# Performance work log

Hardware: AMD Instinct MI355X
Metric: run time of the kernel (lower is better)

## Reference

```python
import jax, jax.numpy as jnp
import numpy as np


def setup_inputs() -> dict:
    key = jax.random.key(0)
    k1, k2 = jax.random.split(key)
    B, N, M, D = 8, 8192, 8192, 3
    preds = jax.random.normal(k1, (B, M, D), dtype=jnp.float32)
    gts = jax.random.normal(k2, (B, N, D), dtype=jnp.float32)
    return {"preds": preds, "gts": gts}


def reference(preds, gts):
    # Faithful to torch: P = batch_pairwise_dist(x=gts, y=preds), shape [B, N_gts, N_preds]
    x = gts.astype(jnp.float32)
    y = preds.astype(jnp.float32)
    xx = jnp.sum(x * x, axis=-1)                      # [B, N]
    yy = jnp.sum(y * y, axis=-1)                      # [B, M]
    zz = jnp.einsum('bnd,bmd->bnm', x, y)             # [B, N, M]
    P = xx[:, :, None] + yy[:, None, :] - 2.0 * zz    # squared distances
    loss_1 = jnp.mean(jnp.min(P, axis=1))             # min over gts points
    loss_2 = jnp.mean(jnp.min(P, axis=2))             # min over pred points
    return loss_1 + loss_2
```

## Files before the change

### kernel.cpp

```cpp
#include <hip/hip_runtime.h>
#include <hip/hip_bf16.h>


typedef _Float16 f16x8 __attribute__((ext_vector_type(8)));
typedef float f32x16 __attribute__((ext_vector_type(16)));

#define NPTS 8192
#define BATCH 8
#define TPB 512
#define BN 512
#define BM 1024
#define CPB 4
#define CTPC (BM / 32)
#define NQ_TOT (2 * BATCH * NPTS)

__device__ __forceinline__ void cvt_split(float v, _Float16& h, _Float16& l) {
    h = (_Float16)v;
    l = (_Float16)(v - (float)h);
}

__global__ __launch_bounds__(TPB, 4) void chamfer_mfma_kernel(
    const float* __restrict__ preds, const float* __restrict__ gts,
    float* __restrict__ partial )
{
    __shared__ f16x8 ldsB[CTPC][2][32];

    const int bid  = blockIdx.x;
    const int pass = bid >> 8;
    const int b       = (bid >> 5) & 7;
    const int rowblk  = (bid >> 1) & 15;
    const int colhalf = bid & 1;

    const float* __restrict__ Asrc = (pass == 0) ? gts : preds;
    const float* __restrict__ Bsrc = (pass == 0) ? preds : gts;
    const float* __restrict__ Ab = Asrc + (size_t)b * NPTS * 3;
    const float* __restrict__ Bb = Bsrc + (size_t)b * NPTS * 3;

    const int tid  = threadIdx.x;
    const int lane = tid & 63;
    const int w    = tid >> 6;
    const int kh   = lane >> 5;
    const int cl   = lane & 31;

    f16x8 af[2];
#pragma unroll
    for (int t = 0; t < 2; ++t) {
        const int row = rowblk * BN + w * 64 + t * 32 + cl;
        const float* xp = Ab + (size_t)row * 3;
        const float x0 = xp[0], x1 = xp[1], x2 = xp[2];
        _Float16 h0, l0, h1, l1, h2, l2;
        cvt_split(x0, h0, l0); cvt_split(x1, h1, l1); cvt_split(x2, h2, l2);
        const float xx = x0 * x0 + x1 * x1 + x2 * x2;
        _Float16 xxh, xxl; cvt_split(xx, xxh, xxl);
        const f16x8 lo = { h0, h1, h2, l0, l1, l2, h0, h1 };
        const f16x8 hi = { h2, (_Float16)1, (_Float16)1, xxh, xxl,
                           (_Float16)0, (_Float16)0, (_Float16)0 };
        af[t] = kh ? hi : lo;
    }

    const f16x8* __restrict__ bptr = &ldsB[0][kh][cl];
    const f32x16 zc = {};

    float rb[2][16];
#pragma unroll
    for (int t = 0; t < 2; ++t)
#pragma unroll
        for (int r = 0; r < 16; ++r) rb[t][r] = 1e30f;

    for (int chunk = 0; chunk < CPB; ++chunk) {
        const int cbase = (colhalf * CPB + chunk) * BM;
        __syncthreads();
#pragma unroll
        for (int i = 0; i < BM / TPB; ++i) {
            const int pl = i * TPB + tid;
            const float* yp = Bb + (size_t)(cbase + pl) * 3;
            const float y0 = yp[0], y1 = yp[1], y2 = yp[2];
            _Float16 nh0, nl0, nh1, nl1, nh2, nl2;
            { const float hf = (float)(_Float16)y0; nh0 = (_Float16)(-2.f * hf); nl0 = (_Float16)(-2.f * (y0 - hf)); }
            { const float hf = (float)(_Float16)y1; nh1 = (_Float16)(-2.f * hf); nl1 = (_Float16)(-2.f * (y1 - hf)); }
            { const float hf = (float)(_Float16)y2; nh2 = (_Float16)(-2.f * hf); nl2 = (_Float16)(-2.f * (y2 - hf)); }
            const float yy = y0 * y0 + y1 * y1 + y2 * y2;
            _Float16 yyh, yyl; cvt_split(yy, yyh, yyl);
            const f16x8 lo = { nh0, nh1, nh2, nh0, nh1, nh2, nl0, nl1 };
            const f16x8 hi = { nl2, yyh, yyl, (_Float16)1, (_Float16)1,
                               (_Float16)0, (_Float16)0, (_Float16)0 };
            ldsB[pl >> 5][0][pl & 31] = lo;
            ldsB[pl >> 5][1][pl & 31] = hi;
        }
        __syncthreads();

#pragma unroll 2
        for (int ct = 0; ct < CTPC; ct += 2) {
            const f16x8 bfA = bptr[ct * 64];
            const f16x8 bfB = bptr[(ct + 1) * 64];
#pragma unroll
            for (int t = 0; t < 2; ++t) {
                const f32x16 aA = __builtin_amdgcn_mfma_f32_32x32x16_f16(af[t], bfA, zc, 0, 0, 0);
                const f32x16 aB = __builtin_amdgcn_mfma_f32_32x32x16_f16(af[t], bfB, zc, 0, 0, 0);
#pragma unroll
                for (int r = 0; r < 16; ++r)
                    rb[t][r] = fminf(fminf(aA[r], aB[r]), rb[t][r]);
            }
        }
    }

#pragma unroll
    for (int t = 0; t < 2; ++t)
#pragma unroll
        for (int r = 0; r < 16; ++r) {
            float v = rb[t][r];
            v = fminf(v, __shfl_xor(v, 1, 64));
            v = fminf(v, __shfl_xor(v, 2, 64));
            v = fminf(v, __shfl_xor(v, 4, 64));
            v = fminf(v, __shfl_xor(v, 8, 64));
            v = fminf(v, __shfl_xor(v, 16, 64));
            rb[t][r] = v;
        }

    if (cl == 0) {
        float* rbase = partial + (((size_t)(pass * BATCH + b) * NPTS)
                     + rowblk * BN + w * 64) * 2 + colhalf;
#pragma unroll
        for (int t = 0; t < 2; ++t)
#pragma unroll
            for (int r = 0; r < 16; ++r) {
                const int rloc = (r & 3) + 8 * (r >> 2) + 4 * kh;
                rbase[(t * 32 + rloc) * 2] = rb[t][r];
            }
    }
}

__global__ __launch_bounds__(256) void chamfer_reduce1(
    const float* __restrict__ partial, float* __restrict__ bsums)
{
    const int gid = blockIdx.x * 256 + threadIdx.x;
    const float2 v = ((const float2*)partial)[gid];
    float m = fminf(v.x, v.y);

#pragma unroll
    for (int off = 32; off > 0; off >>= 1) m += __shfl_down(m, off, 64);

    __shared__ float wsum[4];
    const int lane = threadIdx.x & 63;
    const int wid  = threadIdx.x >> 6;
    if (lane == 0) wsum[wid] = m;
    __syncthreads();
    if (threadIdx.x == 0)
        bsums[blockIdx.x] = (wsum[0] + wsum[1]) + (wsum[2] + wsum[3]);
}

__global__ __launch_bounds__(512) void chamfer_reduce2(
    const float* __restrict__ bsums, float* __restrict__ out)
{
    float m = bsums[threadIdx.x];
#pragma unroll
    for (int off = 32; off > 0; off >>= 1) m += __shfl_down(m, off, 64);

    __shared__ float wsum[8];
    const int lane = threadIdx.x & 63;
    const int wid  = threadIdx.x >> 6;
    if (lane == 0) wsum[wid] = m;
    __syncthreads();
    if (threadIdx.x == 0) {
        float t = ((wsum[0] + wsum[1]) + (wsum[2] + wsum[3]))
                + ((wsum[4] + wsum[5]) + (wsum[6] + wsum[7]));
        out[0] = t * (1.0f / 65536.0f);
    }
}

extern "C" void kernel_launch(void* const* d_in, const int* in_sizes, int n_in,
                              void* d_out, int out_size, void* d_ws, size_t ws_size,
                              hipStream_t stream) {
    const float* preds = (const float*)d_in[0];
    const float* gts   = (const float*)d_in[1];
    float* out = (float*)d_out;

    float* partial = (float*)d_ws;
    float* bsums   = (float*)((char*)d_ws + (size_t)NQ_TOT * 2 * sizeof(float));

    chamfer_mfma_kernel<<<512, TPB, 0, stream>>>(preds, gts, partial);
    chamfer_reduce1<<<512, 256, 0, stream>>>(partial, bsums);
    chamfer_reduce2<<<1, 512, 0, stream>>>(bsums, out);
}
```

Baseline: 45.83 us.

## Swap MFMA operand roles so row-min reduces in-register, double-buffer LDS tiles

Output points are now held in registers as the B operand, and the reduced points stream through LDS as the A operand. Each MFMA output column then reduces with a tree of 16 fminf per tile plus one cross-half shuffle, instead of 16 per-register running minima followed by a 5-step shuffle reduction. The LDS tile is double-buffered: the next chunk's global loads are issued before the current chunk's MFMAs and are written afterwards, so there is one barrier per chunk. The reduction is split four ways, so the partial buffer grows to four entries per query and the first reduce kernel reads float4.

```diff
diff --git a/kernel.cpp b/kernel.cpp
--- a/kernel.cpp
+++ b/kernel.cpp
@@ -8,33 +8,69 @@
 #define NPTS 8192
 #define BATCH 8
 #define TPB 512
-#define BN 512
-#define BM 1024
-#define CPB 4
-#define CTPC (BM / 32)
+#define T_OUT 4
+#define OPB 1024
+#define NRS 4
+#define RED_PER_BLK (NPTS / NRS)
+#define CHUNK 512
+#define NCH (RED_PER_BLK / CHUNK)
+#define ATILES (CHUNK / 32)
 #define NQ_TOT (2 * BATCH * NPTS)
 
 __device__ __forceinline__ void cvt_split(float v, _Float16& h, _Float16& l) {
-    h = (_Float16)v;
-    l = (_Float16)(v - (float)h);
+    h = (_Float16)v; l = (_Float16)(v - (float)h);
+}
+
+__device__ __forceinline__ void aform(float x0, float x1, float x2,
+                                      f16x8& lo, f16x8& hi) {
+    _Float16 h0, l0, h1, l1, h2, l2;
+    cvt_split(x0, h0, l0); cvt_split(x1, h1, l1); cvt_split(x2, h2, l2);
+    const float xx = x0 * x0 + x1 * x1 + x2 * x2;
+    _Float16 xxh, xxl; cvt_split(xx, xxh, xxl);
+    lo = f16x8{ h0, h1, h2, l0, l1, l2, h0, h1 };
+    hi = f16x8{ h2, (_Float16)1, (_Float16)1, xxh, xxl,
+                (_Float16)0, (_Float16)0, (_Float16)0 };
+}
+
+__device__ __forceinline__ void bform(float y0, float y1, float y2,
+                                      f16x8& lo, f16x8& hi) {
+    _Float16 h0, l0, h1, l1, h2, l2;
+    { const float hf = (float)(_Float16)y0; h0 = (_Float16)(-2.f * hf); l0 = (_Float16)(-2.f * (y0 - hf)); }
+    { const float hf = (float)(_Float16)y1; h1 = (_Float16)(-2.f * hf); l1 = (_Float16)(-2.f * (y1 - hf)); }
+    { const float hf = (float)(_Float16)y2; h2 = (_Float16)(-2.f * hf); l2 = (_Float16)(-2.f * (y2 - hf)); }
+    const float yy = y0 * y0 + y1 * y1 + y2 * y2;
+    _Float16 yyh, yyl; cvt_split(yy, yyh, yyl);
+    lo = f16x8{ h0, h1, h2, h0, h1, h2, l0, l1 };
+    hi = f16x8{ l2, yyh, yyl, (_Float16)1, (_Float16)1,
+                (_Float16)0, (_Float16)0, (_Float16)0 };
+}
+
+__device__ __forceinline__ float min16(const f32x16 a) {
+    const float m0 = fminf(a[0], a[1]),   m1 = fminf(a[2], a[3]);
+    const float m2 = fminf(a[4], a[5]),   m3 = fminf(a[6], a[7]);
+    const float m4 = fminf(a[8], a[9]),   m5 = fminf(a[10], a[11]);
+    const float m6 = fminf(a[12], a[13]), m7 = fminf(a[14], a[15]);
+    const float n0 = fminf(m0, m1), n1 = fminf(m2, m3);
+    const float n2 = fminf(m4, m5), n3 = fminf(m6, m7);
+    return fminf(fminf(n0, n1), fminf(n2, n3));
 }
 
 __global__ __launch_bounds__(TPB, 4) void chamfer_mfma_kernel(
     const float* __restrict__ preds, const float* __restrict__ gts,
     float* __restrict__ partial )
 {
-    __shared__ f16x8 ldsB[CTPC][2][32];
+    __shared__ f16x8 ldsA[2][ATILES][2][32];
 
     const int bid  = blockIdx.x;
     const int pass = bid >> 8;
-    const int b       = (bid >> 5) & 7;
-    const int rowblk  = (bid >> 1) & 15;
-    const int colhalf = bid & 1;
+    const int b    = (bid >> 5) & 7;
+    const int ob   = (bid >> 2) & 7;
+    const int rs   = bid & 3;
 
-    const float* __restrict__ Asrc = (pass == 0) ? gts : preds;
-    const float* __restrict__ Bsrc = (pass == 0) ? preds : gts;
-    const float* __restrict__ Ab = Asrc + (size_t)b * NPTS * 3;
-    const float* __restrict__ Bb = Bsrc + (size_t)b * NPTS * 3;
+    const float* __restrict__ Osrc = (pass == 0) ? preds : gts;
+    const float* __restrict__ Rsrc = (pass == 0) ? gts : preds;
+    const float* __restrict__ Ob = Osrc + (size_t)b * NPTS * 3;
+    const float* __restrict__ Rb = Rsrc + (size_t)b * NPTS * 3;
 
     const int tid  = threadIdx.x;
     const int lane = tid & 63;
@@ -42,91 +78,64 @@
     const int kh   = lane >> 5;
     const int cl   = lane & 31;
 
-    f16x8 af[2];
+    f16x8 bf[T_OUT];
 #pragma unroll
-    for (int t = 0; t < 2; ++t) {
-        const int row = rowblk * BN + w * 64 + t * 32 + cl;
-        const float* xp = Ab + (size_t)row * 3;
-        const float x0 = xp[0], x1 = xp[1], x2 = xp[2];
-        _Float16 h0, l0, h1, l1, h2, l2;
-        cvt_split(x0, h0, l0); cvt_split(x1, h1, l1); cvt_split(x2, h2, l2);
-        const float xx = x0 * x0 + x1 * x1 + x2 * x2;
-        _Float16 xxh, xxl; cvt_split(xx, xxh, xxl);
-        const f16x8 lo = { h0, h1, h2, l0, l1, l2, h0, h1 };
-        const f16x8 hi = { h2, (_Float16)1, (_Float16)1, xxh, xxl,
-                           (_Float16)0, (_Float16)0, (_Float16)0 };
-        af[t] = kh ? hi : lo;
+    for (int t = 0; t < T_OUT; ++t) {
+        const int opt = ob * OPB + (w * T_OUT + t) * 32 + cl;
+        const float* yp = Ob + (size_t)opt * 3;
+        f16x8 lo, hi; bform(yp[0], yp[1], yp[2], lo, hi);
+        bf[t] = kh ? hi : lo;
     }
 
-    const f16x8* __restrict__ bptr = &ldsB[0][kh][cl];
     const f32x16 zc = {};
+    float rb0 = 1e30f, rb1 = 1e30f, rb2 = 1e30f, rb3 = 1e30f;
 
-    float rb[2][16];
-#pragma unroll
-    for (int t = 0; t < 2; ++t)
-#pragma unroll
-        for (int r = 0; r < 16; ++r) rb[t][r] = 1e30f;
+    {
+        const float* rp = Rb + (size_t)(rs * RED_PER_BLK + tid) * 3;
+        f16x8 lo, hi; aform(rp[0], rp[1], rp[2], lo, hi);
+        ldsA[0][tid >> 5][0][tid & 31] = lo;
+        ldsA[0][tid >> 5][1][tid & 31] = hi;
+    }
+    __syncthreads();
 
-    for (int chunk = 0; chunk < CPB; ++chunk) {
-        const int cbase = (colhalf * CPB + chunk) * BM;
-        __syncthreads();
-#pragma unroll
-        for (int i = 0; i < BM / TPB; ++i) {
-            const int pl = i * TPB + tid;
-            const float* yp = Bb + (size_t)(cbase + pl) * 3;
-            const float y0 = yp[0], y1 = yp[1], y2 = yp[2];
-            _Float16 nh0, nl0, nh1, nl1, nh2, nl2;
-            { const float hf = (float)(_Float16)y0; nh0 = (_Float16)(-2.f * hf); nl0 = (_Float16)(-2.f * (y0 - hf)); }
-            { const float hf = (float)(_Float16)y1; nh1 = (_Float16)(-2.f * hf); nl1 = (_Float16)(-2.f * (y1 - hf)); }
-            { const float hf = (float)(_Float16)y2; nh2 = (_Float16)(-2.f * hf); nl2 = (_Float16)(-2.f * (y2 - hf)); }
-            const float yy = y0 * y0 + y1 * y1 + y2 * y2;
-            _Float16 yyh, yyl; cvt_split(yy, yyh, yyl);
-            const f16x8 lo = { nh0, nh1, nh2, nh0, nh1, nh2, nl0, nl1 };
-            const f16x8 hi = { nl2, yyh, yyl, (_Float16)1, (_Float16)1,
-                               (_Float16)0, (_Float16)0, (_Float16)0 };
-            ldsB[pl >> 5][0][pl & 31] = lo;
-            ldsB[pl >> 5][1][pl & 31] = hi;
+    for (int c = 0; c < NCH; ++c) {
+        float g0 = 0.f, g1 = 0.f, g2 = 0.f;
+        if (c + 1 < NCH) {
+            const float* rp = Rb + (size_t)(rs * RED_PER_BLK + (c + 1) * CHUNK + tid) * 3;
+            g0 = rp[0]; g1 = rp[1]; g2 = rp[2];
+        }
+
+        const f16x8* __restrict__ abase = &ldsA[c & 1][0][kh][cl];
+#pragma unroll 4
+        for (int at = 0; at < ATILES; ++at) {
+            const f16x8 af = abase[at * 64];
+            const f32x16 a0 = __builtin_amdgcn_mfma_f32_32x32x16_f16(af, bf[0], zc, 0, 0, 0);
+            const f32x16 a1 = __builtin_amdgcn_mfma_f32_32x32x16_f16(af, bf[1], zc, 0, 0, 0);
+            rb0 = fminf(rb0, min16(a0));
+            rb1 = fminf(rb1, min16(a1));
+            const f32x16 a2 = __builtin_amdgcn_mfma_f32_32x32x16_f16(af, bf[2], zc, 0, 0, 0);
+            const f32x16 a3 = __builtin_amdgcn_mfma_f32_32x32x16_f16(af, bf[3], zc, 0, 0, 0);
+            rb2 = fminf(rb2, min16(a2));
+            rb3 = fminf(rb3, min16(a3));
+        }
+
+        if (c + 1 < NCH) {
+            f16x8 lo, hi; aform(g0, g1, g2, lo, hi);
+            ldsA[(c + 1) & 1][tid >> 5][0][tid & 31] = lo;
+            ldsA[(c + 1) & 1][tid >> 5][1][tid & 31] = hi;
         }
         __syncthreads();
-
-#pragma unroll 2
-        for (int ct = 0; ct < CTPC; ct += 2) {
-            const f16x8 bfA = bptr[ct * 64];
-            const f16x8 bfB = bptr[(ct + 1) * 64];
-#pragma unroll
-            for (int t = 0; t < 2; ++t) {
-                const f32x16 aA = __builtin_amdgcn_mfma_f32_32x32x16_f16(af[t], bfA, zc, 0, 0, 0);
-                const f32x16 aB = __builtin_amdgcn_mfma_f32_32x32x16_f16(af[t], bfB, zc, 0, 0, 0);
-#pragma unroll
-                for (int r = 0; r < 16; ++r)
-                    rb[t][r] = fminf(fminf(aA[r], aB[r]), rb[t][r]);
-            }
-        }
     }
 
+    float rbv[T_OUT] = { rb0, rb1, rb2, rb3 };
+    const size_t qbase = (size_t)(pass * BATCH + b) * NPTS;
 #pragma unroll
-    for (int t = 0; t < 2; ++t)
-#pragma unroll
-        for (int r = 0; r < 16; ++r) {
-            float v = rb[t][r];
-            v = fminf(v, __shfl_xor(v, 1, 64));
-            v = fminf(v, __shfl_xor(v, 2, 64));
-            v = fminf(v, __shfl_xor(v, 4, 64));
-            v = fminf(v, __shfl_xor(v, 8, 64));
-            v = fminf(v, __shfl_xor(v, 16, 64));
-            rb[t][r] = v;
+    for (int t = 0; t < T_OUT; ++t) {
+        const float v = fminf(rbv[t], __shfl_xor(rbv[t], 32, 64));
+        if (kh == 0) {
+            const int opt = ob * OPB + (w * T_OUT + t) * 32 + cl;
+            partial[(qbase + opt) * NRS + rs] = v;
         }
-
-    if (cl == 0) {
-        float* rbase = partial + (((size_t)(pass * BATCH + b) * NPTS)
-                     + rowblk * BN + w * 64) * 2 + colhalf;
-#pragma unroll
-        for (int t = 0; t < 2; ++t)
-#pragma unroll
-            for (int r = 0; r < 16; ++r) {
-                const int rloc = (r & 3) + 8 * (r >> 2) + 4 * kh;
-                rbase[(t * 32 + rloc) * 2] = rb[t][r];
-            }
     }
 }
 
@@ -134,8 +143,8 @@
     const float* __restrict__ partial, float* __restrict__ bsums)
 {
     const int gid = blockIdx.x * 256 + threadIdx.x;
-    const float2 v = ((const float2*)partial)[gid];
-    float m = fminf(v.x, v.y);
+    const float4 v = ((const float4*)partial)[gid];
+    float m = fminf(fminf(v.x, v.y), fminf(v.z, v.w));
 
 #pragma unroll
     for (int off = 32; off > 0; off >>= 1) m += __shfl_down(m, off, 64);
@@ -176,7 +185,7 @@
     float* out = (float*)d_out;
 
     float* partial = (float*)d_ws;
-    float* bsums   = (float*)((char*)d_ws + (size_t)NQ_TOT * 2 * sizeof(float));
+    float* bsums   = (float*)((char*)d_ws + (size_t)NQ_TOT * NRS * sizeof(float));
 
     chamfer_mfma_kernel<<<512, TPB, 0, stream>>>(preds, gts, partial);
     chamfer_reduce1<<<512, 256, 0, stream>>>(partial, bsums);
```

New measurement: 57.40 us. 1.25x slower.
